# Kernel tuning notes

Hardware: AMD Instinct MI355X
Metric: run time of the kernel (lower is better)

Reference implementation:

```python
import jax, jax.numpy as jnp
import numpy as np

IN_CH, OUT_CH = 384, 512


def setup_inputs() -> dict:
    key = jax.random.key(0)
    ks = jax.random.split(key, 9)
    B, C, H, W = 8, IN_CH, 48, 48
    s_in = 1.0 / np.sqrt(IN_CH)
    s_out = 1.0 / np.sqrt(OUT_CH)
    return {
        "x": jax.random.normal(ks[0], (B, C, H, W), dtype=jnp.float32),
        "Wq": jax.random.uniform(ks[1], (OUT_CH, IN_CH), jnp.float32, -s_in, s_in),
        "bq": jax.random.uniform(ks[2], (OUT_CH,), jnp.float32, -s_in, s_in),
        "Wk": jax.random.uniform(ks[3], (OUT_CH, IN_CH), jnp.float32, -s_in, s_in),
        "bk": jax.random.uniform(ks[4], (OUT_CH,), jnp.float32, -s_in, s_in),
        "Wv": jax.random.uniform(ks[5], (OUT_CH, IN_CH), jnp.float32, -s_in, s_in),
        "bv": jax.random.uniform(ks[6], (OUT_CH,), jnp.float32, -s_in, s_in),
        "Wo": jax.random.uniform(ks[7], (OUT_CH, OUT_CH), jnp.float32, -s_out, s_out),
        "bo": jax.random.uniform(ks[8], (OUT_CH,), jnp.float32, -s_out, s_out),
    }


def reference(x, Wq, bq, Wk, bk, Wv, bv, Wo, bo):
    B, C, H, W = x.shape
    N = H * W  # number of spatial tokens
    xf = x.reshape(B, C, N)  # [B, C, N]
    # 1x1 convs == per-pixel linear projections
    q = jnp.einsum('oc,bcn->bno', Wq, xf) + bq  # [B, N, O]
    k = jnp.einsum('oc,bcn->bon', Wk, xf) + bk[None, :, None]  # [B, O, N]
    v = jnp.einsum('oc,bcn->bon', Wv, xf) + bv[None, :, None]  # [B, O, N]
    scale = 1.0 / jnp.sqrt(jnp.asarray(Wq.shape[0], x.dtype))
    attn = jax.nn.softmax(jnp.einsum('bno,bom->bnm', q, k) * scale, axis=-1)  # [B, N, N]
    out = jnp.einsum('bom,bnm->bon', v, attn)  # [B, O, N]
    out = jnp.einsum('po,bon->bpn', Wo, out) + bo[None, :, None]
    return out.reshape(B, Wo.shape[0], H, W)
```

## Files before the change

kernel.cpp:

```cpp
#include <hip/hip_runtime.h>
#include <stdint.h>

#define B_    8
#define CIN   384
#define OCH   512
#define NTOK  2304
#define SCALE 0.044194173824159216f

typedef unsigned short u16;
typedef u16   u16x8 __attribute__((ext_vector_type(8)));
typedef short s16x8 __attribute__((ext_vector_type(8)));
typedef float f32x4 __attribute__((ext_vector_type(4)));

__device__ __forceinline__ u16 f2bf(float f) {
    union { uint32_t i; float f; } v; v.f = f;
    uint32_t r = v.i + 0x7fffu + ((v.i >> 16) & 1u);
    return (u16)(r >> 16);
}

typedef __attribute__((address_space(1))) const uint32_t glb_u32;
typedef __attribute__((address_space(3))) uint32_t lds_u32;

__device__ __forceinline__ void gld16(const u16* g, u16* l) {
    __builtin_amdgcn_global_load_lds((glb_u32*)g, (lds_u32*)l, 16, 0, 0);
}

__device__ __forceinline__ size_t baddr(int row, int col, int Kc) {
    return ((size_t)(row >> 4) * (Kc >> 5) + (col >> 5)) * 512
         + (size_t)(((col >> 3) & 3) * 128 + (row & 15) * 8 + (col & 7));
}

__device__ __forceinline__ void mfma_core(const u16* __restrict__ As,
                                          const u16* __restrict__ Bs,
                                          int wm16, int wn16, int lrow, int kq,
                                          f32x4 acc[4][4])
{
    s16x8 a[4], b[4];
#pragma unroll
    for (int i = 0; i < 4; ++i)
        a[i] = *(const s16x8*)(As + (((wm16 + i) * 64) + kq * 16 + lrow) * 8);
#pragma unroll
    for (int j = 0; j < 4; ++j)
        b[j] = *(const s16x8*)(Bs + (((wn16 + j) * 64) + kq * 16 + lrow) * 8);
#pragma unroll
    for (int i = 0; i < 4; ++i)
#pragma unroll
        for (int j = 0; j < 4; ++j)
            acc[i][j] = __builtin_amdgcn_mfma_f32_16x16x32_bf16(a[i], b[j], acc[i][j], 0, 0, 0);
}

template <int MODE, int K>
__device__ __forceinline__ void gemm64_core(
    u16* __restrict__ sm,
    const u16* __restrict__ A, const u16* __restrict__ Bp,
    const float* __restrict__ aux, void* __restrict__ Cout,
    int N, int m0, int n0, float* __restrict__ rsG)
{
    constexpr int NT = K / 32;
    u16* As0 = sm;
    u16* Bs0 = sm + 2048;
    u16* As1 = sm + 4096;
    u16* Bs1 = sm + 6144;

    const int ln = threadIdx.x & 63;
    const int lrow = ln & 15, kq = ln >> 4;

    const int bpr = K >> 5;
    const size_t rstep = (size_t)bpr << 9;
    const u16* pA = A  + (((size_t)(m0 >> 4) * bpr) << 9) + (size_t)(ln << 3);
    const u16* pB = Bp + (((size_t)(n0 >> 4) * bpr) << 9) + (size_t)(ln << 3);

    f32x4 acc[4][4] = {};

#define STAGE8(ga, gb, Ad, Bd)                                             \
    gld16((ga),             (Ad));        gld16((ga) + rstep,     (Ad) + 512);  \
    gld16((ga) + 2 * rstep, (Ad) + 1024); gld16((ga) + 3 * rstep, (Ad) + 1536); \
    gld16((gb),             (Bd));        gld16((gb) + rstep,     (Bd) + 512);  \
    gld16((gb) + 2 * rstep, (Bd) + 1024); gld16((gb) + 3 * rstep, (Bd) + 1536);

    STAGE8(pA, pB, As0, Bs0)

#pragma unroll 1
    for (int kt = 0; kt < NT; kt += 2) {
        STAGE8(pA + 512, pB + 512, As1, Bs1)
        asm volatile("s_waitcnt vmcnt(8)" ::: "memory");
        mfma_core(As0, Bs0, 0, 0, lrow, kq, acc);
        asm volatile("" ::: "memory");
        if (kt + 2 < NT) {
            STAGE8(pA + 1024, pB + 1024, As0, Bs0)
            asm volatile("s_waitcnt vmcnt(8)" ::: "memory");
        } else {
            asm volatile("s_waitcnt vmcnt(0)" ::: "memory");
        }
        mfma_core(As1, Bs1, 0, 0, lrow, kq, acc);
        asm volatile("" ::: "memory");
        pA += 1024; pB += 1024;
    }
#undef STAGE8

    const int offl = ((lrow >> 3) << 7) + (lrow & 7) + (kq << 5);

    if constexpr (MODE == 0) {
        u16* E = (u16*)Cout;
#pragma unroll
        for (int i = 0; i < 4; ++i) {
            u16* Erow = E + ((size_t)((m0 >> 4) + i) * (N >> 5) + (n0 >> 5)) * 512 + offl;
#pragma unroll
            for (int r = 0; r < 4; ++r) {
                float part = 0.f;
#pragma unroll
                for (int j = 0; j < 4; ++j) {
                    float e = __expf(acc[i][j][r] * SCALE);
                    part += e;
                    Erow[(j >> 1) * 512 + ((j & 1) << 8) + r * 8] = f2bf(e);
                }
                part += __shfl_xor(part, 1);
                part += __shfl_xor(part, 2);
                part += __shfl_xor(part, 4);
                part += __shfl_xor(part, 8);
                if (lrow == 0) atomicAdd(&rsG[m0 + i * 16 + kq * 4 + r], part);
            }
        }
    } else if constexpr (MODE == 1) {
        u16* C = (u16*)Cout;
        float bcol[4];
#pragma unroll
        for (int j = 0; j < 4; ++j) bcol[j] = aux[n0 + j * 16 + lrow];
#pragma unroll
        for (int i = 0; i < 4; ++i) {
            u16* Crow = C + ((size_t)((m0 >> 4) + i) * (N >> 5) + (n0 >> 5)) * 512 + offl;
#pragma unroll
            for (int j = 0; j < 4; ++j) {
                u16* Cj = Crow + (j >> 1) * 512 + ((j & 1) << 8);
#pragma unroll
                for (int r = 0; r < 4; ++r)
                    Cj[r * 8] = f2bf(acc[i][j][r] + bcol[j]);
            }
        }
    } else if constexpr (MODE == 2) {
        u16* C = (u16*)Cout;
#pragma unroll
        for (int i = 0; i < 4; ++i) {
            const float4 b4 = *(const float4*)(aux + m0 + i * 16 + kq * 4);
            u16* Crow = C + ((size_t)((m0 >> 4) + i) * (N >> 5) + (n0 >> 5)) * 512 + offl;
#pragma unroll
            for (int j = 0; j < 4; ++j) {
                u16* Cj = Crow + (j >> 1) * 512 + ((j & 1) << 8);
                Cj[0]  = f2bf(acc[i][j][0] + b4.x);
                Cj[8]  = f2bf(acc[i][j][1] + b4.y);
                Cj[16] = f2bf(acc[i][j][2] + b4.z);
                Cj[24] = f2bf(acc[i][j][3] + b4.w);
            }
        }
    } else if constexpr (MODE == 3) {
        u16* C = (u16*)Cout;
#pragma unroll
        for (int i = 0; i < 4; ++i) {
            const float4 rs4 = *(const float4*)(aux + m0 + i * 16 + kq * 4);
            const float inv0 = 1.0f / rs4.x, inv1 = 1.0f / rs4.y;
            const float inv2 = 1.0f / rs4.z, inv3 = 1.0f / rs4.w;
            u16* Crow = C + ((size_t)((m0 >> 4) + i) * (N >> 5) + (n0 >> 5)) * 512 + offl;
#pragma unroll
            for (int j = 0; j < 4; ++j) {
                u16* Cj = Crow + (j >> 1) * 512 + ((j & 1) << 8);
                Cj[0]  = f2bf(acc[i][j][0] * inv0);
                Cj[8]  = f2bf(acc[i][j][1] * inv1);
                Cj[16] = f2bf(acc[i][j][2] * inv2);
                Cj[24] = f2bf(acc[i][j][3] * inv3);
            }
        }
    } else {
        float* C = (float*)Cout;
#pragma unroll
        for (int i = 0; i < 4; ++i) {
            const int row = m0 + i * 16 + kq * 4;
            const float4 b4 = *(const float4*)(aux + row);
            const float bv4[4] = {b4.x, b4.y, b4.z, b4.w};
#pragma unroll
            for (int r = 0; r < 4; ++r)
#pragma unroll
                for (int j = 0; j < 4; ++j)
                    C[(size_t)(row + r) * N + n0 + j * 16 + lrow] = acc[i][j][r] + bv4[r];
        }
    }
}

#define WQKV_SZ (OCH * CIN)
#define WO_SZ   (OCH * OCH)
#define CH_QKV  (WQKV_SZ / 8)
#define CH_WO   (WO_SZ / 8)
#define CH_TOT  (3 * CH_QKV + CH_WO)

__global__ __launch_bounds__(256) void prep_w_kernel(
    const float* __restrict__ Wq, const float* __restrict__ Wk,
    const float* __restrict__ Wv, const float* __restrict__ Wo,
    u16* __restrict__ Wqb, u16* __restrict__ Wkb,
    u16* __restrict__ Wvb, u16* __restrict__ Wob)
{
    int lc = blockIdx.x * 256 + threadIdx.x;
    if (lc >= CH_TOT) return;
    const float* src; u16* dst; int Kc;
    if      (lc < CH_QKV)     { src = Wq; dst = Wqb; Kc = CIN; }
    else if (lc < 2 * CH_QKV) { src = Wk; dst = Wkb; Kc = CIN; lc -= CH_QKV; }
    else if (lc < 3 * CH_QKV) { src = Wv; dst = Wvb; Kc = CIN; lc -= 2 * CH_QKV; }
    else                      { src = Wo; dst = Wob; Kc = OCH; lc -= 3 * CH_QKV; }
    const int brick = lc >> 6, l = lc & 63;
    const int bpr = Kc >> 5;
    const int g = brick / bpr, c = brick % bpr;
    const int row = g * 16 + (l & 15);
    const int col = c * 32 + (l >> 4) * 8;
    const float* s = src + (size_t)row * Kc + col;
    float4 v0 = *(const float4*)s;
    float4 v1 = *(const float4*)(s + 4);
    u16x8 o;
    o[0] = f2bf(v0.x); o[1] = f2bf(v0.y); o[2] = f2bf(v0.z); o[3] = f2bf(v0.w);
    o[4] = f2bf(v1.x); o[5] = f2bf(v1.y); o[6] = f2bf(v1.z); o[7] = f2bf(v1.w);
    *(u16x8*)(dst + (size_t)lc * 8) = o;
}

__global__ __launch_bounds__(256) void transpose_x_kernel(
    const float* __restrict__ x, u16* __restrict__ xT)
{
    const int n0 = blockIdx.x * 64;
    const int c0 = blockIdx.y * 64;
    const int b  = blockIdx.z;
    const float* X = x + (size_t)b * CIN * NTOK;

    __shared__ float Ts[64][66];

    const int t = threadIdx.x;
#pragma unroll
    for (int rep = 0; rep < 4; ++rep) {
        const int cr = (t >> 4) + rep * 16;
        const int n4 = (t & 15) * 4;
        float4 v = *(const float4*)(X + (size_t)(c0 + cr) * NTOK + n0 + n4);
        *(float2*)&Ts[cr][n4]     = make_float2(v.x, v.y);
        *(float2*)&Ts[cr][n4 + 2] = make_float2(v.z, v.w);
    }
    __syncthreads();

    u16* O = xT + (size_t)b * NTOK * CIN;
#pragma unroll
    for (int rep = 0; rep < 2; ++rep) {
        const int nr = (t >> 3) + rep * 32;
        const int c8 = (t & 7) * 8;
        u16 tmp[8];
#pragma unroll
        for (int j = 0; j < 8; ++j) tmp[j] = f2bf(Ts[c8 + j][nr]);
        *(u16x8*)(O + baddr(n0 + nr, c0 + c8, CIN)) = *(const u16x8*)tmp;
    }
}

__global__ __launch_bounds__(64) void qkv64_kernel(
    const u16* __restrict__ xT,
    const u16* __restrict__ Wqb, const float* __restrict__ bq,
    const u16* __restrict__ Wkb, const float* __restrict__ bk,
    const u16* __restrict__ Wvb, const float* __restrict__ bv,
    u16* __restrict__ Qt, u16* __restrict__ Kt, u16* __restrict__ Vw)
{
    __shared__ __align__(16) u16 sm[8192];
    const int sel = blockIdx.x % 24;
    const int b = sel & 7, which = sel >> 3;
    const int rem = blockIdx.x / 24;
    const u16* xTb = xT + (size_t)b * NTOK * CIN;
    if (which < 2) {
        const int n0 = (rem & 7) * 64, m0 = (rem >> 3) * 64;
        gemm64_core<1, CIN>(sm, xTb, which ? Wkb : Wqb, which ? bk : bq,
            (which ? Kt : Qt) + (size_t)b * NTOK * OCH, OCH, m0, n0, nullptr);
    } else {
        const int n0 = (rem % 36) * 64, m0 = (rem / 36) * 64;
        gemm64_core<2, CIN>(sm, Wvb, xTb, bv,
            Vw + (size_t)b * OCH * NTOK, NTOK, m0, n0, nullptr);
    }
}

__global__ __launch_bounds__(64) void logits64_kernel(
    const u16* __restrict__ Qt, const u16* __restrict__ Kt,
    u16* __restrict__ Ew, float* __restrict__ rowsumG)
{
    __shared__ __align__(16) u16 sm[8192];
    const int z = blockIdx.x & 7;
    const int rem = blockIdx.x >> 3;
    const int n0 = (rem % 36) * 64, m0 = (rem / 36) * 64;
    gemm64_core<0, OCH>(sm, Qt + (size_t)z * NTOK * OCH, Kt + (size_t)z * NTOK * OCH,
        nullptr, Ew + (size_t)z * NTOK * NTOK, NTOK, m0, n0,
        rowsumG + (size_t)z * NTOK);
}

__global__ __launch_bounds__(64) void pv64_kernel(
    const u16* __restrict__ Ew, const u16* __restrict__ Vw,
    const float* __restrict__ rowsumG, u16* __restrict__ AOt)
{
    __shared__ __align__(16) u16 sm[8192];
    const int z = blockIdx.x & 7;
    const int rem = blockIdx.x >> 3;
    const int n0 = (rem & 7) * 64, m0 = (rem >> 3) * 64;
    gemm64_core<3, NTOK>(sm, Ew + (size_t)z * NTOK * NTOK, Vw + (size_t)z * OCH * NTOK,
        rowsumG + (size_t)z * NTOK, AOt + (size_t)z * NTOK * OCH, OCH, m0, n0, nullptr);
}

__global__ __launch_bounds__(64) void out64_kernel(
    const u16* __restrict__ Wob, const u16* __restrict__ AOt,
    const float* __restrict__ bo, float* __restrict__ out)
{
    __shared__ __align__(16) u16 sm[8192];
    const int z = blockIdx.x & 7;
    const int rem = blockIdx.x >> 3;
    const int n0 = (rem % 36) * 64, m0 = (rem / 36) * 64;
    gemm64_core<4, OCH>(sm, Wob, AOt + (size_t)z * NTOK * OCH, bo,
        out + (size_t)z * OCH * NTOK, NTOK, m0, n0, nullptr);
}

extern "C" void kernel_launch(void* const* d_in, const int* in_sizes, int n_in,
                              void* d_out, int out_size, void* d_ws, size_t ws_size,
                              hipStream_t stream)
{
    const float* x  = (const float*)d_in[0];
    const float* Wq = (const float*)d_in[1];
    const float* bq = (const float*)d_in[2];
    const float* Wk = (const float*)d_in[3];
    const float* bk = (const float*)d_in[4];
    const float* Wv = (const float*)d_in[5];
    const float* bv = (const float*)d_in[6];
    const float* Wo = (const float*)d_in[7];
    const float* bo = (const float*)d_in[8];
    float* out = (float*)d_out;

    u16* ws = (u16*)d_ws;
    u16* Wqb = ws;
    u16* Wkb = Wqb + WQKV_SZ;
    u16* Wvb = Wkb + WQKV_SZ;
    u16* Wob = Wvb + WQKV_SZ;
    u16* xT  = Wob + WO_SZ;
    const size_t xtsz  = (size_t)B_ * NTOK * CIN;
    const size_t qkvsz = (size_t)B_ * NTOK * OCH;
    u16* Qt  = xT + xtsz;
    u16* Kt  = Qt + qkvsz;
    u16* Vw  = Kt + qkvsz;
    u16* Ew  = Vw + qkvsz;
    float* rowsumG = (float*)(Ew + (size_t)B_ * NTOK * NTOK);
    u16* AOt = Qt;

    dim3 blk(256), blk64(64);

    prep_w_kernel<<<dim3((CH_TOT + 255) / 256), blk, 0, stream>>>(
        Wq, Wk, Wv, Wo, Wqb, Wkb, Wvb, Wob);
    transpose_x_kernel<<<dim3(NTOK / 64, CIN / 64, B_), blk, 0, stream>>>(x, xT);
    hipMemsetAsync(rowsumG, 0, (size_t)B_ * NTOK * sizeof(float), stream);

    qkv64_kernel<<<dim3(288 * 24), blk64, 0, stream>>>(
        xT, Wqb, bq, Wkb, bk, Wvb, bv, Qt, Kt, Vw);

    logits64_kernel<<<dim3(1296 * 8), blk64, 0, stream>>>(Qt, Kt, Ew, rowsumG);

    pv64_kernel<<<dim3(288 * 8), blk64, 0, stream>>>(Ew, Vw, rowsumG, AOt);

    out64_kernel<<<dim3(288 * 8), blk64, 0, stream>>>(Wob, AOt, bo, out);
}
```

Before: 295.2 us.

## Use 128x128 four-wave tiles for logits-exp kernel with LDS rowsum reduction

Replaces the 64x64 single-wave logits GEMM with a 256-thread kernel computing 128x128 tiles, each wave owning a 64x64 quadrant. This halves global traffic per output for Q and K and cuts global rowsum atomics by reducing partial sums in shared memory first. The new loop is single-buffered with two barriers per k-step and no load/compute overlap, which may expose memory latency compared with the old double-buffered pipeline.

```diff
diff --git a/kernel.cpp b/kernel.cpp
--- a/kernel.cpp
+++ b/kernel.cpp
@@ -30,6 +30,23 @@
          + (size_t)(((col >> 3) & 3) * 128 + (row & 15) * 8 + (col & 7));
 }
 
+__device__ __forceinline__ void stage_blocked(const u16* __restrict__ base,
+                                              int row0, int k0, int Kc,
+                                              u16* __restrict__ dst, int t)
+{
+    const int lane = t & 63;
+    const int w = t >> 6;
+    const int bpr = Kc >> 5;
+#pragma unroll
+    for (int it = 0; it < 2; ++it) {
+        const int ck = w * 2 + it;
+        const u16* gp = base + ((size_t)((row0 >> 4) + ck) * bpr + (k0 >> 5)) * 512
+                      + (size_t)lane * 8;
+        u16* lp = dst + ck * 512;
+        __builtin_amdgcn_global_load_lds((glb_u32*)gp, (lds_u32*)lp, 16, 0, 0);
+    }
+}
+
 __device__ __forceinline__ void mfma_core(const u16* __restrict__ As,
                                           const u16* __restrict__ Bs,
                                           int wm16, int wn16, int lrow, int kq,
@@ -54,7 +71,7 @@
     u16* __restrict__ sm,
     const u16* __restrict__ A, const u16* __restrict__ Bp,
     const float* __restrict__ aux, void* __restrict__ Cout,
-    int N, int m0, int n0, float* __restrict__ rsG)
+    int N, int m0, int n0)
 {
     constexpr int NT = K / 32;
     u16* As0 = sm;
@@ -100,28 +117,7 @@
 
     const int offl = ((lrow >> 3) << 7) + (lrow & 7) + (kq << 5);
 
-    if constexpr (MODE == 0) {
-        u16* E = (u16*)Cout;
-#pragma unroll
-        for (int i = 0; i < 4; ++i) {
-            u16* Erow = E + ((size_t)((m0 >> 4) + i) * (N >> 5) + (n0 >> 5)) * 512 + offl;
-#pragma unroll
-            for (int r = 0; r < 4; ++r) {
-                float part = 0.f;
-#pragma unroll
-                for (int j = 0; j < 4; ++j) {
-                    float e = __expf(acc[i][j][r] * SCALE);
-                    part += e;
-                    Erow[(j >> 1) * 512 + ((j & 1) << 8) + r * 8] = f2bf(e);
-                }
-                part += __shfl_xor(part, 1);
-                part += __shfl_xor(part, 2);
-                part += __shfl_xor(part, 4);
-                part += __shfl_xor(part, 8);
-                if (lrow == 0) atomicAdd(&rsG[m0 + i * 16 + kq * 4 + r], part);
-            }
-        }
-    } else if constexpr (MODE == 1) {
+    if constexpr (MODE == 1) {
         u16* C = (u16*)Cout;
         float bcol[4];
 #pragma unroll
@@ -266,25 +262,69 @@
     if (which < 2) {
         const int n0 = (rem & 7) * 64, m0 = (rem >> 3) * 64;
         gemm64_core<1, CIN>(sm, xTb, which ? Wkb : Wqb, which ? bk : bq,
-            (which ? Kt : Qt) + (size_t)b * NTOK * OCH, OCH, m0, n0, nullptr);
+            (which ? Kt : Qt) + (size_t)b * NTOK * OCH, OCH, m0, n0);
     } else {
         const int n0 = (rem % 36) * 64, m0 = (rem / 36) * 64;
         gemm64_core<2, CIN>(sm, Wvb, xTb, bv,
-            Vw + (size_t)b * OCH * NTOK, NTOK, m0, n0, nullptr);
-    }
-}
-
-__global__ __launch_bounds__(64) void logits64_kernel(
+            Vw + (size_t)b * OCH * NTOK, NTOK, m0, n0);
+    }
+}
+
+__global__ __launch_bounds__(256) void logits_exp_kernel(
     const u16* __restrict__ Qt, const u16* __restrict__ Kt,
     u16* __restrict__ Ew, float* __restrict__ rowsumG)
 {
-    __shared__ __align__(16) u16 sm[8192];
-    const int z = blockIdx.x & 7;
-    const int rem = blockIdx.x >> 3;
-    const int n0 = (rem % 36) * 64, m0 = (rem / 36) * 64;
-    gemm64_core<0, OCH>(sm, Qt + (size_t)z * NTOK * OCH, Kt + (size_t)z * NTOK * OCH,
-        nullptr, Ew + (size_t)z * NTOK * NTOK, NTOK, m0, n0,
-        rowsumG + (size_t)z * NTOK);
+    const int z   = blockIdx.x % B_;
+    const int rem = blockIdx.x / B_;
+    const int n0 = (rem % (NTOK / 128)) * 128;
+    const int m0 = (rem / (NTOK / 128)) * 128;
+    const u16* A  = Qt + (size_t)z * NTOK * OCH;
+    const u16* Bp = Kt + (size_t)z * NTOK * OCH;
+
+    __shared__ u16 As[128 * 32];
+    __shared__ u16 Bs[128 * 32];
+    __shared__ float rowsumL[128];
+
+    const int t = threadIdx.x;
+    const int w = t >> 6, ln = t & 63;
+    const int wm16 = (w & 1) * 4, wn16 = (w >> 1) * 4;
+    const int lrow = ln & 15, kq = ln >> 4;
+
+    if (t < 128) rowsumL[t] = 0.f;
+
+    f32x4 acc[4][4] = {};
+
+    for (int k0 = 0; k0 < OCH; k0 += 32) {
+        stage_blocked(A, m0, k0, OCH, As, t);
+        stage_blocked(Bp, n0, k0, OCH, Bs, t);
+        __syncthreads();
+        mfma_core(As, Bs, wm16, wn16, lrow, kq, acc);
+        __syncthreads();
+    }
+
+    u16* E = Ew + (size_t)z * NTOK * NTOK;
+    const int offl = ((lrow >> 3) << 7) + (lrow & 7) + (kq << 5);
+#pragma unroll
+    for (int i = 0; i < 4; ++i) {
+        u16* Erow = E + ((size_t)((m0 >> 4) + wm16 + i) * (NTOK >> 5) + (n0 >> 5)) * 512 + offl;
+#pragma unroll
+        for (int r = 0; r < 4; ++r) {
+            float part = 0.f;
+#pragma unroll
+            for (int j = 0; j < 4; ++j) {
+                float e = __expf(acc[i][j][r] * SCALE);
+                part += e;
+                Erow[((wn16 + j) >> 1) * 512 + ((j & 1) << 8) + r * 8] = f2bf(e);
+            }
+            part += __shfl_xor(part, 1);
+            part += __shfl_xor(part, 2);
+            part += __shfl_xor(part, 4);
+            part += __shfl_xor(part, 8);
+            if (lrow == 0) atomicAdd(&rowsumL[(wm16 + i) * 16 + kq * 4 + r], part);
+        }
+    }
+    __syncthreads();
+    if (t < 128) atomicAdd(&rowsumG[(size_t)z * NTOK + m0 + t], rowsumL[t]);
 }
 
 __global__ __launch_bounds__(64) void pv64_kernel(
@@ -296,7 +336,7 @@
     const int rem = blockIdx.x >> 3;
     const int n0 = (rem & 7) * 64, m0 = (rem >> 3) * 64;
     gemm64_core<3, NTOK>(sm, Ew + (size_t)z * NTOK * NTOK, Vw + (size_t)z * OCH * NTOK,
-        rowsumG + (size_t)z * NTOK, AOt + (size_t)z * NTOK * OCH, OCH, m0, n0, nullptr);
+        rowsumG + (size_t)z * NTOK, AOt + (size_t)z * NTOK * OCH, OCH, m0, n0);
 }
 
 __global__ __launch_bounds__(64) void out64_kernel(
@@ -308,7 +348,7 @@
     const int rem = blockIdx.x >> 3;
     const int n0 = (rem % 36) * 64, m0 = (rem / 36) * 64;
     gemm64_core<4, OCH>(sm, Wob, AOt + (size_t)z * NTOK * OCH, bo,
-        out + (size_t)z * OCH * NTOK, NTOK, m0, n0, nullptr);
+        out + (size_t)z * OCH * NTOK, NTOK, m0, n0);
 }
 
 extern "C" void kernel_launch(void* const* d_in, const int* in_sizes, int n_in,
@@ -351,7 +391,7 @@
     qkv64_kernel<<<dim3(288 * 24), blk64, 0, stream>>>(
         xT, Wqb, bq, Wkb, bk, Wvb, bv, Qt, Kt, Vw);
 
-    logits64_kernel<<<dim3(1296 * 8), blk64, 0, stream>>>(Qt, Kt, Ew, rowsumG);
+    logits_exp_kernel<<<dim3(18 * 18 * B_), blk, 0, stream>>>(Qt, Kt, Ew, rowsumG);
 
     pv64_kernel<<<dim3(288 * 8), blk64, 0, stream>>>(Ew, Vw, rowsumG, AOt);
 
```

New measurement: 286.7 us. -2.9%, faster.
